# Kernel tuning notes

Measured on AMD Instinct MI355X. Metric: run time of the kernel, lower is better.

The kernel has to match this reference:

```python
import jax, jax.numpy as jnp
import numpy as np

D_MODEL = 1024
D_FFN = 4096
N_HEAD = 16
D_K = D_MODEL // N_HEAD
EPS = 1e-10


def _layernorm(x, gamma, beta):
    mean = jnp.mean(x, axis=-1, keepdims=True)
    var = jnp.mean((x - mean) ** 2, axis=-1, keepdims=True)
    return gamma * ((x - mean) / jnp.sqrt(var + EPS)) + beta


def setup_inputs() -> dict:
    key = jax.random.key(0)
    ks = jax.random.split(key, 16)
    s = 1.0 / np.sqrt(D_MODEL)
    sf = 1.0 / np.sqrt(D_FFN)
    return {
        "x": jax.random.normal(ks[0], (4, 2048, D_MODEL), jnp.float32),
        "wq": jax.random.uniform(ks[1], (D_MODEL, D_MODEL), jnp.float32, -s, s),
        "bq": jnp.zeros((D_MODEL,), jnp.float32),
        "wk": jax.random.uniform(ks[2], (D_MODEL, D_MODEL), jnp.float32, -s, s),
        "bk": jnp.zeros((D_MODEL,), jnp.float32),
        "wv": jax.random.uniform(ks[3], (D_MODEL, D_MODEL), jnp.float32, -s, s),
        "bv": jnp.zeros((D_MODEL,), jnp.float32),
        "wo": jax.random.uniform(ks[4], (D_MODEL, D_MODEL), jnp.float32, -s, s),
        "bo": jnp.zeros((D_MODEL,), jnp.float32),
        "g1": jnp.ones((D_MODEL,), jnp.float32),
        "b1": jnp.zeros((D_MODEL,), jnp.float32),
        "w1": jax.random.uniform(ks[5], (D_MODEL, D_FFN), jnp.float32, -s, s),
        "bf1": jnp.zeros((D_FFN,), jnp.float32),
        "w2": jax.random.uniform(ks[6], (D_FFN, D_MODEL), jnp.float32, -sf, sf),
        "bf2": jnp.zeros((D_MODEL,), jnp.float32),
        "g2": jnp.ones((D_MODEL,), jnp.float32),
        "b2": jnp.zeros((D_MODEL,), jnp.float32),
    }


def reference(x, wq, bq, wk, bk, wv, bv, wo, bo, g1, b1, w1, bf1, w2, bf2, g2, b2):
    B, S, _ = x.shape
    # projections -> (B, H, S, d_k)
    q = (x @ wq + bq).reshape(B, S, N_HEAD, D_K).transpose(0, 2, 1, 3)
    k = (x @ wk + bk).reshape(B, S, N_HEAD, D_K).transpose(0, 2, 1, 3)
    v = (x @ wv + bv).reshape(B, S, N_HEAD, D_K).transpose(0, 2, 1, 3)
    score = jnp.einsum("bhqd,bhkd->bhqk", q, k) / jnp.sqrt(jnp.asarray(D_K, x.dtype))
    attn = jax.nn.softmax(score, axis=-1)
    out = jnp.einsum("bhqk,bhkd->bhqd", attn, v)
    out = out.transpose(0, 2, 1, 3).reshape(B, S, D_MODEL)
    out = out @ wo + bo
    out1 = _layernorm(x + out, g1, b1)
    # FFN (dropout is identity in eval mode)
    ff = jax.nn.relu(out1 @ w1 + bf1) @ w2 + bf2
    out2 = _layernorm(out1 + ff, g2, b2)
    return (out2, attn)
```

## Files before the change

kernel.cpp:

```cpp
#include <hip/hip_runtime.h>
#include <hip/hip_bf16.h>

#define DEV __device__ __forceinline__

typedef __attribute__((ext_vector_type(4))) float f32x4;
typedef __attribute__((ext_vector_type(8))) __bf16 bf16v;
typedef __attribute__((ext_vector_type(8))) unsigned short u16x8;
typedef __attribute__((ext_vector_type(4))) unsigned short u16x4;

DEV unsigned short f2b(float x) {
    unsigned u = __builtin_bit_cast(unsigned, x);
    unsigned r = u + 0x7FFF + ((u >> 16) & 1);
    return (unsigned short)(r >> 16);
}
DEV float b2f(unsigned short u) {
    unsigned v = (unsigned)u << 16;
    return __builtin_bit_cast(float, v);
}

DEV void gl_lds16(const void* g, void* l) {
    __builtin_amdgcn_global_load_lds(
        (const __attribute__((address_space(1))) unsigned*)g,
        (__attribute__((address_space(3))) unsigned*)l,
        16, 0, 0);
}


DEV void transp_dev(const float* __restrict__ in, unsigned short* __restrict__ out,
                    int R, int C, int bx, int by, float (*t)[33]) {
    int tx = threadIdx.x & 31, ty = threadIdx.x >> 5;
    long c0 = (long)bx * 32, r0 = (long)by * 32;
#pragma unroll
    for (int i = 0; i < 4; i++)
        t[ty + i * 8][tx] = in[(r0 + ty + i * 8) * C + c0 + tx];
    __syncthreads();
#pragma unroll
    for (int i = 0; i < 4; i++)
        out[(c0 + ty + i * 8) * R + r0 + tx] = f2b(t[tx][ty + i * 8]);
}

__global__ __launch_bounds__(256) void prep_all(
    const float* __restrict__ x, const float* __restrict__ wq,
    const float* __restrict__ wk, const float* __restrict__ wv,
    const float* __restrict__ wo, const float* __restrict__ w1,
    const float* __restrict__ w2, const float* __restrict__ bq,
    const float* __restrict__ bk, const float* __restrict__ bv,
    unsigned short* __restrict__ xb, unsigned short* __restrict__ wqkvT,
    unsigned short* __restrict__ woT, unsigned short* __restrict__ w1T,
    unsigned short* __restrict__ w2T, float* __restrict__ bqkv) {
    __shared__ float t[32][33];
    int id = blockIdx.x;
    if (id < 8192) {
        long i = ((long)id * 256 + threadIdx.x) * 4;
        float4 f = *(const float4*)(x + i);
        u16x4 u;
        u[0] = f2b(f.x); u[1] = f2b(f.y); u[2] = f2b(f.z); u[3] = f2b(f.w);
        *(u16x4*)(xb + i) = u;
        return;
    }
    id -= 8192;
    if (id < 1024) { transp_dev(wq, wqkvT, 1024, 1024, id & 31, id >> 5, t); return; }
    id -= 1024;
    if (id < 1024) { transp_dev(wk, wqkvT + 1048576, 1024, 1024, id & 31, id >> 5, t); return; }
    id -= 1024;
    if (id < 1024) { transp_dev(wv, wqkvT + 2097152, 1024, 1024, id & 31, id >> 5, t); return; }
    id -= 1024;
    if (id < 1024) { transp_dev(wo, woT, 1024, 1024, id & 31, id >> 5, t); return; }
    id -= 1024;
    if (id < 4096) { transp_dev(w1, w1T, 1024, 4096, id & 127, id >> 7, t); return; }
    id -= 4096;
    if (id < 4096) { transp_dev(w2, w2T, 4096, 1024, id & 31, id >> 5, t); return; }
    id -= 4096;
    int i = id * 256 + threadIdx.x;
    float v = (i < 1024) ? bq[i] : (i < 2048) ? bk[i - 1024] : bv[i - 2048];
    bqkv[i] = v;
}

DEV float waveSum(float v) {
#pragma unroll
    for (int o = 32; o > 0; o >>= 1) v += __shfl_xor(v, o);
    return v;
}

__global__ __launch_bounds__(256) void ln_rows(const float* __restrict__ in,
                                               const float* __restrict__ g,
                                               const float* __restrict__ b,
                                               float* __restrict__ outF,
                                               unsigned short* __restrict__ outB) {
    const float* p = in + (long)blockIdx.x * 1024;
    __shared__ float red[4], red2[4];
    int t = threadIdx.x, lane = t & 63, wave = t >> 6;
    float4 v = ((const float4*)p)[t];
    float s = v.x + v.y + v.z + v.w;
    float q = v.x * v.x + v.y * v.y + v.z * v.z + v.w * v.w;
    s = waveSum(s); q = waveSum(q);
    if (lane == 0) { red[wave] = s; red2[wave] = q; }
    __syncthreads();
    s = red[0] + red[1] + red[2] + red[3];
    q = red2[0] + red2[1] + red2[2] + red2[3];
    float mean = s * (1.0f / 1024.0f);
    float var = q * (1.0f / 1024.0f) - mean * mean;
    float rstd = rsqrtf(var + 1e-10f);
    float4 gg = ((const float4*)g)[t];
    float4 bb = ((const float4*)b)[t];
    float4 o;
    o.x = gg.x * ((v.x - mean) * rstd) + bb.x;
    o.y = gg.y * ((v.y - mean) * rstd) + bb.y;
    o.z = gg.z * ((v.z - mean) * rstd) + bb.z;
    o.w = gg.w * ((v.w - mean) * rstd) + bb.w;
    if (outF) ((float4*)(outF + (long)blockIdx.x * 1024))[t] = o;
    if (outB) {
        u16x4 u;
        u[0] = f2b(o.x); u[1] = f2b(o.y); u[2] = f2b(o.z); u[3] = f2b(o.w);
        *(u16x4*)(outB + (long)blockIdx.x * 1024 + (long)t * 4) = u;
    }
}

__global__ __launch_bounds__(256, 2) void attn_fused(
    const unsigned short* __restrict__ qb,
    const unsigned short* __restrict__ kb,
    const unsigned short* __restrict__ vt,
    float* __restrict__ attn,
    unsigned short* __restrict__ ao) {
    __shared__ __align__(16) char smem[65536];
    __shared__ float sredM[4][16], sredS[4][16];

    int id = blockIdx.x;
    int swz = (id & 7) * 1024 + (id >> 3);
    const int z = swz >> 7;
    const int m0 = (swz & 127) * 16;

    const int tid = threadIdx.x, lane = tid & 63, w = tid >> 6;
    const int g = lane >> 4, l15 = lane & 15;

    const char* qz = (const char*)(qb + (long)z * 131072);
    const char* kz = (const char*)(kb + (long)z * 131072);
    const char* vz = (const char*)(vt + (long)z * 131072);

    const char* qrow = qz + (long)(m0 + l15) * 128;
    bf16v aq0 = *(const bf16v*)(qrow + g * 16);
    bf16v aq1 = *(const bf16v*)(qrow + 64 + g * 16);

    f32x4 acc[8][4];
#pragma unroll
    for (int c = 0; c < 8; c++)
#pragma unroll
        for (int t = 0; t < 4; t++) acc[c][t] = (f32x4)(0.0f);

    const int soff = ((lane & 7) * 16) ^ (((lane >> 3) & 7) << 4);

    auto stage = [&](int c) {
        const char* src = kz + (long)(c * 256 + w * 8 + (lane >> 3)) * 128 + soff;
        char* dst = smem + (c & 1) * 32768 + w * 1024;
#pragma unroll
        for (int i = 0; i < 8; ++i)
            gl_lds16(src + (long)i * 4096, dst + i * 4096);
    };

    stage(0);
    for (int c = 0; c < 8; ++c) {
        if (c < 7) {
            stage(c + 1);
            asm volatile("s_waitcnt vmcnt(8)" ::: "memory");
        } else {
            asm volatile("s_waitcnt vmcnt(0)" ::: "memory");
        }
        __builtin_amdgcn_sched_barrier(0);
        __builtin_amdgcn_s_barrier();
        const char* base = smem + (c & 1) * 32768;
#pragma unroll
        for (int t = 0; t < 4; ++t) {
            const int row = w * 64 + t * 16 + l15;
            const char* bp = base + row * 128;
            const int sw = (lane & 7) << 4;
            bf16v bk0 = *(const bf16v*)(bp + ((g * 16) ^ sw));
            bf16v bk1 = *(const bf16v*)(bp + ((64 + g * 16) ^ sw));
            acc[c][t] = __builtin_amdgcn_mfma_f32_16x16x32_bf16(aq0, bk0, acc[c][t], 0, 0, 0);
            acc[c][t] = __builtin_amdgcn_mfma_f32_16x16x32_bf16(aq1, bk1, acc[c][t], 0, 0, 0);
        }
        __builtin_amdgcn_s_barrier();
    }

    float M[4], S[4];
#pragma unroll
    for (int j = 0; j < 4; ++j) {
        float m = -1e30f;
#pragma unroll
        for (int c = 0; c < 8; c++)
#pragma unroll
            for (int t = 0; t < 4; t++) m = fmaxf(m, acc[c][t][j]);
        m = fmaxf(m, __shfl_xor(m, 1));
        m = fmaxf(m, __shfl_xor(m, 2));
        m = fmaxf(m, __shfl_xor(m, 4));
        m = fmaxf(m, __shfl_xor(m, 8));
        M[j] = m;
    }
    if (l15 == 0) {
        sredM[w][g * 4 + 0] = M[0];
        sredM[w][g * 4 + 1] = M[1];
        sredM[w][g * 4 + 2] = M[2];
        sredM[w][g * 4 + 3] = M[3];
    }
    __syncthreads();
#pragma unroll
    for (int j = 0; j < 4; ++j) {
        int r = g * 4 + j;
        M[j] = 0.125f * fmaxf(fmaxf(sredM[0][r], sredM[1][r]),
                              fmaxf(sredM[2][r], sredM[3][r]));
        S[j] = 0.0f;
    }
#pragma unroll
    for (int c = 0; c < 8; c++)
#pragma unroll
        for (int t = 0; t < 4; t++) {
            f32x4 v = acc[c][t];
            v[0] = __expf(v[0] * 0.125f - M[0]);
            v[1] = __expf(v[1] * 0.125f - M[1]);
            v[2] = __expf(v[2] * 0.125f - M[2]);
            v[3] = __expf(v[3] * 0.125f - M[3]);
            acc[c][t] = v;
            S[0] += v[0]; S[1] += v[1]; S[2] += v[2]; S[3] += v[3];
        }
#pragma unroll
    for (int j = 0; j < 4; ++j) {
        float s = S[j];
        s += __shfl_xor(s, 1);
        s += __shfl_xor(s, 2);
        s += __shfl_xor(s, 4);
        s += __shfl_xor(s, 8);
        S[j] = s;
    }
    if (l15 == 0) {
        sredS[w][g * 4 + 0] = S[0];
        sredS[w][g * 4 + 1] = S[1];
        sredS[w][g * 4 + 2] = S[2];
        sredS[w][g * 4 + 3] = S[3];
    }
    __syncthreads();
    float inv[4];
#pragma unroll
    for (int j = 0; j < 4; ++j) {
        int r = g * 4 + j;
        inv[j] = 1.0f / (sredS[0][r] + sredS[1][r] + sredS[2][r] + sredS[3][r]);
    }

    float* ab = attn + (long)z * 4194304 + (long)m0 * 2048;
#pragma unroll
    for (int c = 0; c < 8; c++)
#pragma unroll
        for (int t = 0; t < 4; t++) {
            const int col = c * 256 + w * 64 + t * 16 + l15;
#pragma unroll
            for (int j = 0; j < 4; ++j) {
                const int r = g * 4 + j;
                float p = acc[c][t][j] * inv[j];
                ab[(long)r * 2048 + col] = p;
                *(unsigned short*)(smem + r * 4096 + ((col * 2) ^ ((r & 7) << 4))) = f2b(p);
            }
        }
    __syncthreads();

    f32x4 o0 = (f32x4)(0.0f), o1 = (f32x4)(0.0f);
    f32x4 o2 = (f32x4)(0.0f), o3 = (f32x4)(0.0f);
    const char* vtile = vz + (long)(w * 16 + l15) * 4096;
    const char* prow = smem + l15 * 4096;
    const int psw = (l15 & 7) << 4;
#pragma unroll 4
    for (int ks = 0; ks < 64; ks += 4) {
        bf16v pa0 = *(const bf16v*)(prow + (((ks + 0) * 64 + g * 16) ^ psw));
        bf16v pa1 = *(const bf16v*)(prow + (((ks + 1) * 64 + g * 16) ^ psw));
        bf16v pa2 = *(const bf16v*)(prow + (((ks + 2) * 64 + g * 16) ^ psw));
        bf16v pa3 = *(const bf16v*)(prow + (((ks + 3) * 64 + g * 16) ^ psw));
        bf16v bv0 = *(const bf16v*)(vtile + (ks + 0) * 64 + g * 16);
        bf16v bv1 = *(const bf16v*)(vtile + (ks + 1) * 64 + g * 16);
        bf16v bv2 = *(const bf16v*)(vtile + (ks + 2) * 64 + g * 16);
        bf16v bv3 = *(const bf16v*)(vtile + (ks + 3) * 64 + g * 16);
        o0 = __builtin_amdgcn_mfma_f32_16x16x32_bf16(pa0, bv0, o0, 0, 0, 0);
        o1 = __builtin_amdgcn_mfma_f32_16x16x32_bf16(pa1, bv1, o1, 0, 0, 0);
        o2 = __builtin_amdgcn_mfma_f32_16x16x32_bf16(pa2, bv2, o2, 0, 0, 0);
        o3 = __builtin_amdgcn_mfma_f32_16x16x32_bf16(pa3, bv3, o3, 0, 0, 0);
    }
    o0 = o0 + o1 + o2 + o3;

    const int b = z >> 4, h = z & 15;
    const long tokbase = (long)b * 2048 + m0 + g * 4;
#pragma unroll
    for (int j = 0; j < 4; ++j)
        ao[(tokbase + j) * 1024 + h * 64 + w * 16 + l15] = f2b(o0[j]);
}


enum { M_QKV3 = 0, M_RES = 1, M_RESB = 2, M_RELU = 3 };

struct GArgs {
    const unsigned short* A;
    long lda;
    const unsigned short* B;
    long ldb;
    const float* bias;
    const float* resid;
    const unsigned short* residB;
    float* outF;
    unsigned short* outB;
    unsigned short* outB2;
    unsigned short* outB3;
    long ldo;
    int K;
};

template <int BM, int BN, int WR, int WC, int MODE>
__global__ __launch_bounds__(256) void gemm_k(GArgs g) {
    constexpr int MI = BM / (WR * 16), NI = BN / (WC * 16);
    __shared__ __align__(16) char sm[(BM + BN) * 128];
    char* sA = sm;
    char* sB = sm + BM * 128;
    const int tid = threadIdx.x, lane = tid & 63, wave = tid >> 6;
    const int wr = wave / WC, wc = wave % WC;
    const long m0 = (long)blockIdx.x * BM, n0 = (long)blockIdx.y * BN;

    const char* Ab = (const char*)(g.A + m0 * g.lda);
    const char* Bb = (const char*)(g.B + n0 * g.ldb);
    const long lda = g.lda, ldb = g.ldb;

    f32x4 acc[MI][NI];
#pragma unroll
    for (int mi = 0; mi < MI; mi++)
#pragma unroll
        for (int ni = 0; ni < NI; ni++) acc[mi][ni] = (f32x4)(0.0f);

    for (int k0 = 0; k0 < g.K; k0 += 64) {
#pragma unroll
        for (int i = 0; i < BM / 32; i++) {
            int c = i * 4 + wave;
            int p = c * 1024 + lane * 16;
            int row = p >> 7;
            int scb = (p & 127) ^ ((row & 7) << 4);
            gl_lds16(Ab + (long)row * (lda * 2) + (long)k0 * 2 + scb, sA + c * 1024);
        }
#pragma unroll
        for (int i = 0; i < BN / 32; i++) {
            int c = i * 4 + wave;
            int p = c * 1024 + lane * 16;
            int row = p >> 7;
            int scb = (p & 127) ^ ((row & 7) << 4);
            gl_lds16(Bb + (long)row * (ldb * 2) + (long)k0 * 2 + scb, sB + c * 1024);
        }
        __syncthreads();
#pragma unroll
        for (int ks = 0; ks < 2; ++ks) {
            const int cb = ks * 64 + (lane >> 4) * 16;
            bf16v af[MI], bfv[NI];
#pragma unroll
            for (int mi = 0; mi < MI; mi++) {
                int r = wr * (BM / WR) + mi * 16 + (lane & 15);
                af[mi] = *(const bf16v*)(sA + r * 128 + (cb ^ ((r & 7) << 4)));
            }
#pragma unroll
            for (int ni = 0; ni < NI; ni++) {
                int r = wc * (BN / WC) + ni * 16 + (lane & 15);
                bfv[ni] = *(const bf16v*)(sB + r * 128 + (cb ^ ((r & 7) << 4)));
            }
#pragma unroll
            for (int mi = 0; mi < MI; mi++)
#pragma unroll
                for (int ni = 0; ni < NI; ni++)
                    acc[mi][ni] = __builtin_amdgcn_mfma_f32_16x16x32_bf16(
                        af[mi], bfv[ni], acc[mi][ni], 0, 0, 0);
        }
        __syncthreads();
    }

#pragma unroll
    for (int mi = 0; mi < MI; mi++)
#pragma unroll
        for (int ni = 0; ni < NI; ni++) {
            if constexpr (MODE == M_QKV3) {
                long r = m0 + wr * (BM / WR) + mi * 16 + (lane >> 4) * 4;
                long c = n0 + wc * (BN / WC) + ni * 16 + (lane & 15);
                long b = r >> 11, s = r & 2047;
                float bi = g.bias[c];
                if (c < 2048) {
                    unsigned short* dst = (c < 1024) ? g.outB : g.outB2;
                    long h = (c >> 6) & 15, d = c & 63;
                    long base = ((b * 16 + h) * 2048 + s) * 64 + d;
#pragma unroll
                    for (int j = 0; j < 4; ++j)
                        dst[base + (long)j * 64] = f2b(acc[mi][ni][j] + bi);
                } else {
                    long h = (c - 2048) >> 6, d = c & 63;
                    u16x4 u;
#pragma unroll
                    for (int j = 0; j < 4; ++j) u[j] = f2b(acc[mi][ni][j] + bi);
                    *(u16x4*)(g.outB3 + (b * 16 + h) * 131072 + d * 2048 + s) = u;
                }
            } else {
#pragma unroll
                for (int j = 0; j < 4; ++j) {
                    long r = m0 + wr * (BM / WR) + mi * 16 + (lane >> 4) * 4 + j;
                    long c = n0 + wc * (BN / WC) + ni * 16 + (lane & 15);
                    float v = acc[mi][ni][j];
                    if constexpr (MODE == M_RES) {
                        long i = r * g.ldo + c;
                        g.outF[i] = v + g.bias[c] + g.resid[i];
                    } else if constexpr (MODE == M_RESB) {
                        long i = r * g.ldo + c;
                        g.outF[i] = v + g.bias[c] + b2f(g.residB[i]);
                    } else {
                        float t = v + g.bias[c];
                        g.outB[r * g.ldo + c] = f2b(t > 0.0f ? t : 0.0f);
                    }
                }
            }
        }
}


extern "C" void kernel_launch(void* const* d_in, const int* in_sizes, int n_in,
                              void* d_out, int out_size, void* d_ws, size_t ws_size,
                              hipStream_t stream) {
    const float* x = (const float*)d_in[0];
    const float* wq = (const float*)d_in[1];
    const float* bq = (const float*)d_in[2];
    const float* wk = (const float*)d_in[3];
    const float* bk = (const float*)d_in[4];
    const float* wv = (const float*)d_in[5];
    const float* bv = (const float*)d_in[6];
    const float* wo = (const float*)d_in[7];
    const float* bo = (const float*)d_in[8];
    const float* g1 = (const float*)d_in[9];
    const float* b1 = (const float*)d_in[10];
    const float* w1 = (const float*)d_in[11];
    const float* bf1 = (const float*)d_in[12];
    const float* w2 = (const float*)d_in[13];
    const float* bf2 = (const float*)d_in[14];
    const float* g2 = (const float*)d_in[15];
    const float* b2 = (const float*)d_in[16];

    float* out2 = (float*)d_out;
    float* attn = (float*)d_out + 8388608;

    char* ws = (char*)d_ws;
    size_t off = 0;
    auto alc = [&](size_t bytes) { size_t r = off; off += (bytes + 255) & ~(size_t)255; return r; };

    unsigned short* xb    = (unsigned short*)(ws + alc(16777216));
    unsigned short* wqkvT = (unsigned short*)(ws + alc(6291456));
    unsigned short* woT   = (unsigned short*)(ws + alc(2097152));
    unsigned short* w1T   = (unsigned short*)(ws + alc(8388608));
    unsigned short* w2T   = (unsigned short*)(ws + alc(8388608));
    float* bqkv           = (float*)(ws + alc(12288));
    size_t bigOff = alc(67108864);
    unsigned short* qb = (unsigned short*)(ws + bigOff);
    unsigned short* kb = qb + 8388608;
    unsigned short* vt = kb + 8388608;
    unsigned short* ff1 = qb;
    size_t aoOff = alc(16777216);
    unsigned short* ao  = (unsigned short*)(ws + aoOff);
    unsigned short* o1b = ao;
    size_t rOff = alc(33554432);
    float* r1 = (float*)(ws + rOff);
    float* r2 = r1;

    prep_all<<<20492, 256, 0, stream>>>(x, wq, wk, wv, wo, w1, w2, bq, bk, bv,
                                        xb, wqkvT, woT, w1T, w2T, bqkv);

    {
        GArgs a{};
        a.A = xb; a.lda = 1024; a.B = wqkvT; a.ldb = 1024; a.K = 1024;
        a.bias = bqkv; a.outB = qb; a.outB2 = kb; a.outB3 = vt;
        gemm_k<128, 128, 2, 2, M_QKV3><<<dim3(64, 24), 256, 0, stream>>>(a);
    }
    attn_fused<<<8192, 256, 0, stream>>>(qb, kb, vt, attn, ao);
    {
        GArgs a{};
        a.A = ao; a.lda = 1024; a.B = woT; a.ldb = 1024;
        a.bias = bo; a.resid = x; a.outF = r1; a.ldo = 1024; a.K = 1024;
        gemm_k<128, 128, 2, 2, M_RES><<<dim3(64, 8), 256, 0, stream>>>(a);
    }
    ln_rows<<<8192, 256, 0, stream>>>(r1, g1, b1, nullptr, o1b);
    {
        GArgs a{};
        a.A = o1b; a.lda = 1024; a.B = w1T; a.ldb = 1024;
        a.bias = bf1; a.outB = ff1; a.ldo = 4096; a.K = 1024;
        gemm_k<128, 128, 2, 2, M_RELU><<<dim3(64, 32), 256, 0, stream>>>(a);
    }
    {
        GArgs a{};
        a.A = ff1; a.lda = 4096; a.B = w2T; a.ldb = 4096;
        a.bias = bf2; a.residB = o1b; a.outF = r2; a.ldo = 1024; a.K = 4096;
        gemm_k<128, 128, 2, 2, M_RESB><<<dim3(64, 8), 256, 0, stream>>>(a);
    }
    ln_rows<<<8192, 256, 0, stream>>>(r2, g2, b2, out2, nullptr);

    (void)in_sizes; (void)n_in; (void)out_size; (void)ws_size;
}
```

Measured before the change: 875.5 us.

## Add 256x256 double-buffered GEMM kernel for QKV and FFN1 projections

```diff
diff --git a/kernel.cpp b/kernel.cpp
--- a/kernel.cpp
+++ b/kernel.cpp
@@ -308,6 +308,131 @@
     int K;
 };
 
+template <int MODE>
+__global__ __launch_bounds__(512, 1) void gemm256(GArgs g) {
+    __shared__ __align__(16) char smem[131072];
+    const int tid = threadIdx.x, lane = tid & 63, wave = tid >> 6;
+    const int wr = wave >> 2, wc = wave & 3;
+    const int g2 = lane >> 4, l15 = lane & 15;
+    const long m0 = (long)blockIdx.x * 256, n0 = (long)blockIdx.y * 256;
+    const char* Ab = (const char*)(g.A + m0 * g.lda);
+    const char* Bb = (const char*)(g.B + n0 * g.ldb);
+    const long lda2 = g.lda * 2, ldb2 = g.ldb * 2;
+
+    f32x4 acc[8][4];
+#pragma unroll
+    for (int mi = 0; mi < 8; mi++)
+#pragma unroll
+        for (int ni = 0; ni < 4; ni++) acc[mi][ni] = (f32x4)(0.0f);
+
+    auto stage = [&](int t) {
+        const int buf = (t & 1) * 32768;
+        const long k0b = (long)t * 128;
+#pragma unroll
+        for (int i = 0; i < 4; ++i) {
+            int c = i * 8 + wave;
+            int p = c * 1024 + lane * 16;
+            int row = p >> 7;
+            int scb = (p & 127) ^ ((row & 7) << 4);
+            gl_lds16(Ab + (long)row * lda2 + k0b + scb, smem + buf + c * 1024);
+        }
+#pragma unroll
+        for (int i = 0; i < 4; ++i) {
+            int c = i * 8 + wave;
+            int p = c * 1024 + lane * 16;
+            int row = p >> 7;
+            int scb = (p & 127) ^ ((row & 7) << 4);
+            gl_lds16(Bb + (long)row * ldb2 + k0b + scb, smem + 65536 + buf + c * 1024);
+        }
+    };
+
+    const int NT = g.K >> 6;
+    stage(0);
+    for (int t = 0; t < NT; ++t) {
+        if (t + 1 < NT) {
+            stage(t + 1);
+            asm volatile("s_waitcnt vmcnt(8)" ::: "memory");
+        } else {
+            asm volatile("s_waitcnt vmcnt(0)" ::: "memory");
+        }
+        __builtin_amdgcn_sched_barrier(0);
+        __builtin_amdgcn_s_barrier();
+        const char* bufA = smem + (t & 1) * 32768;
+        const char* bufB = smem + 65536 + (t & 1) * 32768;
+        bf16v bfr[4][2];
+#pragma unroll
+        for (int ni = 0; ni < 4; ++ni) {
+            int r = wc * 64 + ni * 16 + l15;
+            const char* bp = bufB + r * 128;
+            int sw = (r & 7) << 4;
+            bfr[ni][0] = *(const bf16v*)(bp + ((g2 * 16) ^ sw));
+            bfr[ni][1] = *(const bf16v*)(bp + ((64 + g2 * 16) ^ sw));
+        }
+#pragma unroll
+        for (int q = 0; q < 4; ++q) {
+            bf16v af[2][2];
+#pragma unroll
+            for (int u = 0; u < 2; ++u) {
+                int r = wr * 128 + (q * 2 + u) * 16 + l15;
+                const char* ap = bufA + r * 128;
+                int sw = (r & 7) << 4;
+                af[u][0] = *(const bf16v*)(ap + ((g2 * 16) ^ sw));
+                af[u][1] = *(const bf16v*)(ap + ((64 + g2 * 16) ^ sw));
+            }
+            asm volatile("s_waitcnt lgkmcnt(0)" ::: "memory");
+            __builtin_amdgcn_sched_barrier(0);
+            __builtin_amdgcn_s_setprio(1);
+#pragma unroll
+            for (int u = 0; u < 2; ++u)
+#pragma unroll
+                for (int ni = 0; ni < 4; ++ni) {
+                    acc[q * 2 + u][ni] = __builtin_amdgcn_mfma_f32_16x16x32_bf16(
+                        af[u][0], bfr[ni][0], acc[q * 2 + u][ni], 0, 0, 0);
+                    acc[q * 2 + u][ni] = __builtin_amdgcn_mfma_f32_16x16x32_bf16(
+                        af[u][1], bfr[ni][1], acc[q * 2 + u][ni], 0, 0, 0);
+                }
+            __builtin_amdgcn_s_setprio(0);
+        }
+        __builtin_amdgcn_sched_barrier(0);
+        __builtin_amdgcn_s_barrier();
+    }
+
+#pragma unroll
+    for (int mi = 0; mi < 8; mi++)
+#pragma unroll
+        for (int ni = 0; ni < 4; ni++) {
+            if constexpr (MODE == M_QKV3) {
+                long r = m0 + wr * 128 + mi * 16 + g2 * 4;
+                long c = n0 + wc * 64 + ni * 16 + l15;
+                long b = r >> 11, s = r & 2047;
+                float bi = g.bias[c];
+                if (c < 2048) {
+                    unsigned short* dst = (c < 1024) ? g.outB : g.outB2;
+                    long h = (c >> 6) & 15, d = c & 63;
+                    long base = ((b * 16 + h) * 2048 + s) * 64 + d;
+#pragma unroll
+                    for (int j = 0; j < 4; ++j)
+                        dst[base + (long)j * 64] = f2b(acc[mi][ni][j] + bi);
+                } else {
+                    long h = (c - 2048) >> 6, d = c & 63;
+                    u16x4 u;
+#pragma unroll
+                    for (int j = 0; j < 4; ++j) u[j] = f2b(acc[mi][ni][j] + bi);
+                    *(u16x4*)(g.outB3 + (b * 16 + h) * 131072 + d * 2048 + s) = u;
+                }
+            } else {
+#pragma unroll
+                for (int j = 0; j < 4; ++j) {
+                    long r = m0 + wr * 128 + mi * 16 + g2 * 4 + j;
+                    long c = n0 + wc * 64 + ni * 16 + l15;
+                    float tv = acc[mi][ni][j] + g.bias[c];
+                    g.outB[r * g.ldo + c] = f2b(tv > 0.0f ? tv : 0.0f);
+                }
+            }
+        }
+}
+
+
 template <int BM, int BN, int WR, int WC, int MODE>
 __global__ __launch_bounds__(256) void gemm_k(GArgs g) {
     constexpr int MI = BM / (WR * 16), NI = BN / (WC * 16);
@@ -374,41 +499,20 @@
     for (int mi = 0; mi < MI; mi++)
 #pragma unroll
         for (int ni = 0; ni < NI; ni++) {
-            if constexpr (MODE == M_QKV3) {
-                long r = m0 + wr * (BM / WR) + mi * 16 + (lane >> 4) * 4;
+#pragma unroll
+            for (int j = 0; j < 4; ++j) {
+                long r = m0 + wr * (BM / WR) + mi * 16 + (lane >> 4) * 4 + j;
                 long c = n0 + wc * (BN / WC) + ni * 16 + (lane & 15);
-                long b = r >> 11, s = r & 2047;
-                float bi = g.bias[c];
-                if (c < 2048) {
-                    unsigned short* dst = (c < 1024) ? g.outB : g.outB2;
-                    long h = (c >> 6) & 15, d = c & 63;
-                    long base = ((b * 16 + h) * 2048 + s) * 64 + d;
-#pragma unroll
-                    for (int j = 0; j < 4; ++j)
-                        dst[base + (long)j * 64] = f2b(acc[mi][ni][j] + bi);
+                float v = acc[mi][ni][j];
+                if constexpr (MODE == M_RES) {
+                    long i = r * g.ldo + c;
+                    g.outF[i] = v + g.bias[c] + g.resid[i];
+                } else if constexpr (MODE == M_RESB) {
+                    long i = r * g.ldo + c;
+                    g.outF[i] = v + g.bias[c] + b2f(g.residB[i]);
                 } else {
-                    long h = (c - 2048) >> 6, d = c & 63;
-                    u16x4 u;
-#pragma unroll
-                    for (int j = 0; j < 4; ++j) u[j] = f2b(acc[mi][ni][j] + bi);
-                    *(u16x4*)(g.outB3 + (b * 16 + h) * 131072 + d * 2048 + s) = u;
-                }
-            } else {
-#pragma unroll
-                for (int j = 0; j < 4; ++j) {
-                    long r = m0 + wr * (BM / WR) + mi * 16 + (lane >> 4) * 4 + j;
-                    long c = n0 + wc * (BN / WC) + ni * 16 + (lane & 15);
-                    float v = acc[mi][ni][j];
-                    if constexpr (MODE == M_RES) {
-                        long i = r * g.ldo + c;
-                        g.outF[i] = v + g.bias[c] + g.resid[i];
-                    } else if constexpr (MODE == M_RESB) {
-                        long i = r * g.ldo + c;
-                        g.outF[i] = v + g.bias[c] + b2f(g.residB[i]);
-                    } else {
-                        float t = v + g.bias[c];
-                        g.outB[r * g.ldo + c] = f2b(t > 0.0f ? t : 0.0f);
-                    }
+                    float t = v + g.bias[c];
+                    g.outB[r * g.ldo + c] = f2b(t > 0.0f ? t : 0.0f);
                 }
             }
         }
@@ -468,7 +572,7 @@
         GArgs a{};
         a.A = xb; a.lda = 1024; a.B = wqkvT; a.ldb = 1024; a.K = 1024;
         a.bias = bqkv; a.outB = qb; a.outB2 = kb; a.outB3 = vt;
-        gemm_k<128, 128, 2, 2, M_QKV3><<<dim3(64, 24), 256, 0, stream>>>(a);
+        gemm256<M_QKV3><<<dim3(32, 12), 512, 0, stream>>>(a);
     }
     attn_fused<<<8192, 256, 0, stream>>>(qb, kb, vt, attn, ao);
     {
@@ -482,7 +586,7 @@
         GArgs a{};
         a.A = o1b; a.lda = 1024; a.B = w1T; a.ldb = 1024;
         a.bias = bf1; a.outB = ff1; a.ldo = 4096; a.K = 1024;
-        gemm_k<128, 128, 2, 2, M_RELU><<<dim3(64, 32), 256, 0, stream>>>(a);
+        gemm256<M_RELU><<<dim3(32, 16), 512, 0, stream>>>(a);
     }
     {
         GArgs a{};
```

Result: faster. 842.5 us (-3.8%).
